# Performance work log

Measured on AMD Instinct MI355X. Metric: run time of the kernel, lower is better.

## Reference

```python
import jax, jax.numpy as jnp
import numpy as np

EMO = 1024
FEAT = 1024
K = 128  # aggregation_k
H_LIST = (4, 8, 16)
D_LIST = tuple(EMO // h for h in H_LIST)  # (256, 128, 64)
D_SUM = sum(D_LIST)  # 448
H_SUM = sum(H_LIST)  # 28
N = len(H_LIST)      # 3 subspaces
TEMP = float(np.power(D_SUM, 0.5))


def _block_mask(sizes, total):
    m = np.zeros((len(sizes), total), np.float32)
    off = 0
    for i, s in enumerate(sizes):
        m[i, off:off + s] = 1.0
        off += s
    return jnp.asarray(m)

M_Q_BLK = _block_mask(D_LIST, D_SUM)  # [N, d_sum]
M_V_BLK = _block_mask(H_LIST, H_SUM)  # [N, h_sum]


def setup_inputs() -> dict:
    key = jax.random.key(0)
    ks = iter(jax.random.split(key, 32))
    nrm = lambda shape, s=1.0: jax.random.normal(next(ks), shape, jnp.float32) * s
    B, Lt, Lp, Nv = 32, 1024, 512, 256
    return {
        "emo_embedding": nrm((B, Lt, EMO)),
        "phr_feat": nrm((B, Lp, FEAT)),
        "video_feat": nrm((B, Nv, FEAT)),
        "w_v_W": nrm((FEAT, FEAT), FEAT ** -0.5), "w_v_b": nrm((FEAT,), 0.01),
        "agg_a_W": nrm((FEAT, K), FEAT ** -0.5), "agg_a_b": nrm((K,), 0.01),
        "agg_c_W": nrm((FEAT, EMO), FEAT ** -0.5), "agg_c_b": nrm((EMO,), 0.01),
        "ele_W": nrm((2 * EMO, 1), (2 * EMO) ** -0.5), "ele_b": nrm((1,), 0.01),
        "wq_W": nrm((EMO, D_SUM), EMO ** -0.5), "wq_b": nrm((D_SUM,), 0.01),
        "wk_W": nrm((EMO, D_SUM), EMO ** -0.5), "wk_b": nrm((D_SUM,), 0.01),
        "wv_W": nrm((EMO, H_SUM), EMO ** -0.5), "wv_b": nrm((H_SUM,), 0.01),
        "wr_W": nrm((EMO, N), EMO ** -0.5), "wr_b": nrm((N,), 0.01),
    }


def reference(emo_embedding, phr_feat, video_feat,
              w_v_W, w_v_b, agg_a_W, agg_a_b, agg_c_W, agg_c_b,
              ele_W, ele_b, wq_W, wq_b, wk_W, wk_b, wv_W, wv_b, wr_W, wr_b):
    B, Lt, _ = emo_embedding.shape
    Nv = video_feat.shape[1]
    Lp = phr_feat.shape[1]

    # --- feature_aggregation ---
    # AdaptiveAvgPool1d(Nv); Lp % Nv == 0 so it is an exact reshape-mean.
    phr = phr_feat.reshape(B, Nv, Lp // Nv, FEAT).mean(axis=2)
    combine = jnp.concatenate([phr @ w_v_W + w_v_b, video_feat], axis=1)   # [B, 2*Nv, FEAT]
    attn_a = jax.nn.softmax(combine @ agg_a_W + agg_a_b, axis=-1)          # [B, 2*Nv, K]
    agg_feat = jnp.einsum('bmk,bme->bke', attn_a, combine @ agg_c_W + agg_c_b)  # [B, K, EMO]

    # --- element_routing ---
    A_pool = jnp.einsum('ble,bke->blk', emo_embedding, agg_feat).mean(axis=1)   # [B, K]
    route = jnp.einsum('bk,bke->be', A_pool, agg_feat)[:, None, :]              # [B, 1, EMO]
    route = jnp.broadcast_to(route, emo_embedding.shape)
    R_e = jnp.tanh(jnp.concatenate([emo_embedding, route], axis=-1) @ ele_W + ele_b)  # [B, Lt, 1]
    route_emo = R_e * emo_embedding                                              # [B, Lt, EMO]

    # --- subspace_routing ---
    Q = route_emo @ wq_W + wq_b        # [B, Lt, d_sum]
    Kp = agg_feat @ wk_W + wk_b        # [B, K, d_sum]
    V = agg_feat @ wv_W + wv_b         # [B, K, h_sum]
    Rp = agg_feat @ wr_W + wr_b        # [B, K, N]

    # N masked copies of Q (block subspace masks); K/R are plain repeats, V is masked.
    Qm = (Q[:, None] * M_Q_BLK[None, :, None, :]).reshape(B, N * Lt, D_SUM)
    Kf = jnp.tile(Kp, (1, N, 1))                                         # [B, N*K, d_sum]
    Vf = (V[:, None] * M_V_BLK[None, :, None, :]).reshape(B, N * K, H_SUM)
    Rf = jnp.tile(Rp, (1, N, 1))                                         # [B, N*K, N]

    attn = jax.nn.softmax(jnp.einsum('bqd,bkd->bqk', Qm, Kf) / TEMP, axis=-1)  # [B, N*Lt, N*K]
    O = jnp.tanh(attn @ Vf).reshape(B, N, Lt, H_SUM)
    O_R = (attn @ Rf).reshape(B, N, Lt, N)

    # per-subspace head gating of route_emo
    T_list = []
    hoff = 0
    for i in range(N):
        hi, di = H_LIST[i], D_LIST[i]
        ori = route_emo.reshape(B, Lt, hi, di)
        Oi = O[:, i, :, hoff:hoff + hi][..., None]      # [B, Lt, hi, 1]
        T_list.append((ori * Oi).reshape(B, Lt, EMO))
        hoff += hi
    T = jnp.stack(T_list, axis=1)                        # [B, N, Lt, EMO]

    Rdiag = jnp.stack([O_R[:, j, :, j].mean(axis=-1) for j in range(N)], axis=1)  # [B, N]
    gate = jax.nn.softmax(Rdiag, axis=-1)[:, :, None, None]
    return emo_embedding + (gate * T).sum(axis=1)
```

## Files before the change

kernel.cpp:

```cpp
#include <hip/hip_runtime.h>
#include <math.h>

typedef long long i64;
typedef __attribute__((ext_vector_type(8))) short bf16x8;
typedef __attribute__((ext_vector_type(4))) float f32x4;

#define TEMP_ISQ 0.047245559f

__device__ __forceinline__ unsigned short f2b(float x) {
  union { float f; unsigned u; } a; a.f = x;
  return (unsigned short)((a.u + 0x7fffu + ((a.u >> 16) & 1u)) >> 16);
}
__device__ __forceinline__ float b2f(unsigned short b) {
  union { float f; unsigned u; } a; a.u = ((unsigned)b) << 16; return a.f;
}

template<int BIAS, int OUTM, int RS, int BZDIV, int XMODE = 0, int SMEPI = 0>
__global__ __launch_bounds__(256)
void gemm_mfma(const unsigned short* __restrict__ Ab, i64 sA,
               const unsigned short* __restrict__ Bb, i64 sB,
               const float* __restrict__ bias,
               void* __restrict__ Ob, i64 sO,
               unsigned short* __restrict__ O2b, i64 sO2,
               int Nn, int Kd, int ldA, int ldB, int ldO,
               const float* __restrict__ rowScale, i64 sRS,
               const float* __restrict__ rsAdd)
{
  __shared__ unsigned short As[2][4096];
  __shared__ unsigned short Bs[2][4096];
  const int tid = threadIdx.x;
  const int w = tid >> 6, lane = tid & 63;

  const int gx = gridDim.x, gy = gridDim.y;
  int nwg = gx * gy * gridDim.z;
  int bid = blockIdx.x + gx * (blockIdx.y + gy * blockIdx.z);
  int L = bid;
  if ((nwg & 7) == 0) L = (bid & 7) * (nwg >> 3) + (bid >> 3);
  const int bx = L % gx;
  int rem = L / gx;
  const int by = rem % gy;
  const int z  = rem / gy;

  const int m0 = by * 128, n0 = bx * 128;
  int zA = (XMODE == 2) ? z / 3 : z;
  const unsigned short* A;
  const unsigned short* B;
  int KdL = Kd;
  if (XMODE == 3) {
    int bb = z / 3, ii = z - bb * 3;
    const int dof_[3] = {0, 256, 384};
    const int kdt_[3] = {256, 128, 64};
    A = Ab + (i64)bb * sA + dof_[ii];
    B = Bb + dof_[ii];
    KdL = kdt_[ii];
  } else if (XMODE == 2) {
    A = Ab + (i64)zA * sA;
    B = Bb + (i64)z * sB;
  } else {
    A = Ab + (i64)z * sA;
    B = Bb + (i64)(BZDIV == 1 ? z : z / BZDIV) * sB;
  }
  const int wr = w >> 1, wc = w & 1;
  const int rS = tid >> 2, sS = tid & 3;
  const int cL = lane & 15, sl = lane >> 4;

  f32x4 acc[4][4];
  #pragma unroll
  for (int i = 0; i < 4; ++i)
    #pragma unroll
    for (int j = 0; j < 4; ++j) acc[i][j] = (f32x4){0.f, 0.f, 0.f, 0.f};

  auto STAGE = [&](int buf, int k0) {
    #pragma unroll
    for (int q = 0; q < 2; ++q) {
      int r = rS + q * 64;
      int sg = sS ^ ((r >> 1) & 3);
      const unsigned short* sa = A + (i64)(m0 + r) * ldA + k0 + sg * 8;
      const unsigned short* sb = B + (i64)(n0 + r) * ldB + k0 + sg * 8;
      __builtin_amdgcn_global_load_lds(
          (__attribute__((address_space(1))) void*)sa,
          (__attribute__((address_space(3))) void*)&As[buf][r * 32 + sS * 8], 16, 0, 0);
      __builtin_amdgcn_global_load_lds(
          (__attribute__((address_space(1))) void*)sb,
          (__attribute__((address_space(3))) void*)&Bs[buf][r * 32 + sS * 8], 16, 0, 0);
    }
  };

  STAGE(0, 0);
  __syncthreads();

  for (int k0 = 0; k0 < KdL; k0 += 32) {
    const int cur = (k0 >> 5) & 1;
    if (k0 + 32 < KdL) STAGE(cur ^ 1, k0 + 32);
    bf16x8 af[4], bfv[4];
    #pragma unroll
    for (int mi = 0; mi < 4; ++mi) {
      int rr = wr * 64 + mi * 16 + cL;
      int ph = sl ^ ((rr >> 1) & 3);
      af[mi] = *(const bf16x8*)&As[cur][rr * 32 + ph * 8];
    }
    #pragma unroll
    for (int ni = 0; ni < 4; ++ni) {
      int rr = wc * 64 + ni * 16 + cL;
      int ph = sl ^ ((rr >> 1) & 3);
      bfv[ni] = *(const bf16x8*)&Bs[cur][rr * 32 + ph * 8];
    }
    #pragma unroll
    for (int mi = 0; mi < 4; ++mi)
      #pragma unroll
      for (int ni = 0; ni < 4; ++ni)
        acc[mi][ni] = __builtin_amdgcn_mfma_f32_16x16x32_bf16(af[mi], bfv[ni], acc[mi][ni], 0, 0, 0);
    __syncthreads();
  }

  const float* bp = (XMODE == 2) ? (bias + (i64)z * 128) : bias;

  if constexpr (SMEPI != 0) {
    const float scale = (SMEPI == 1) ? TEMP_ISQ : 1.f;
    #pragma unroll
    for (int mi = 0; mi < 4; ++mi)
      #pragma unroll
      for (int ni = 0; ni < 4; ++ni)
        #pragma unroll
        for (int rg = 0; rg < 4; ++rg) {
          float v = acc[mi][ni][rg];
          if (RS) v *= tanhf(rowScale[(i64)zA * sRS + m0 + wr * 64 + mi * 16 + sl * 4 + rg] + rsAdd[zA]);
          if (BIAS == 1) v += bp[wc * 64 + ni * 16 + cL];
          acc[mi][ni][rg] = v * scale;
        }
    __shared__ float smax[2][128];
    __shared__ float ssum[2][128];
    #pragma unroll
    for (int mi = 0; mi < 4; ++mi)
      #pragma unroll
      for (int rg = 0; rg < 4; ++rg) {
        float m = fmaxf(fmaxf(acc[mi][0][rg], acc[mi][1][rg]),
                        fmaxf(acc[mi][2][rg], acc[mi][3][rg]));
        #pragma unroll
        for (int o = 1; o < 16; o <<= 1) m = fmaxf(m, __shfl_xor(m, o));
        if (cL == 0) smax[wc][wr * 64 + mi * 16 + sl * 4 + rg] = m;
      }
    __syncthreads();
    #pragma unroll
    for (int mi = 0; mi < 4; ++mi)
      #pragma unroll
      for (int rg = 0; rg < 4; ++rg) {
        int r = wr * 64 + mi * 16 + sl * 4 + rg;
        float m = fmaxf(smax[0][r], smax[1][r]);
        float s = 0.f;
        #pragma unroll
        for (int ni = 0; ni < 4; ++ni) s += expf(acc[mi][ni][rg] - m);
        #pragma unroll
        for (int o = 1; o < 16; o <<= 1) s += __shfl_xor(s, o);
        if (cL == 0) ssum[wc][r] = s;
      }
    __syncthreads();
    unsigned short* OP = (unsigned short*)Ob + (i64)z * sO;
    #pragma unroll
    for (int mi = 0; mi < 4; ++mi)
      #pragma unroll
      for (int rg = 0; rg < 4; ++rg) {
        int r = wr * 64 + mi * 16 + sl * 4 + rg;
        float m = fmaxf(smax[0][r], smax[1][r]);
        float inv = 1.f / (ssum[0][r] + ssum[1][r]);
        #pragma unroll
        for (int ni = 0; ni < 4; ++ni) {
          int c = wc * 64 + ni * 16 + cL;
          unsigned short pv = f2b(expf(acc[mi][ni][rg] - m) * inv);
          if (SMEPI == 1) OP[(i64)(m0 + r) * ldO + c] = pv;
          else            OP[(i64)c * ldO + (m0 + r)] = pv;
        }
      }
    return;
  } else {
    #pragma unroll
    for (int mi = 0; mi < 4; ++mi) {
      const int rowb = m0 + wr * 64 + mi * 16 + sl * 4;
      #pragma unroll
      for (int ni = 0; ni < 4; ++ni) {
        const int col = n0 + wc * 64 + ni * 16 + cL;
        if (col < Nn) {
          float bc = (BIAS == 1) ? bp[col] : 0.f;
          #pragma unroll
          for (int rg = 0; rg < 4; ++rg) {
            float v = acc[mi][ni][rg];
            if (RS) v *= tanhf(rowScale[(i64)zA * sRS + rowb + rg] + rsAdd[zA]);
            v += bc;
            if (BIAS == 2) v += bias[rowb + rg];
            i64 oidx = (i64)(rowb + rg) * ldO + col;
            if (OUTM == 0)      ((float*)Ob)[(i64)z * sO + oidx] = v;
            else if (OUTM == 1) ((unsigned short*)Ob)[(i64)z * sO + oidx] = f2b(v);
            else if (OUTM == 3) ((float*)Ob)[(i64)z * sO + oidx] = tanhf(v * (1.f / 3.f));
            else if (OUTM == 4) {
              float ov = (col < 28) ? tanhf(v * (1.f / 3.f)) : v * (1.f / 1024.f);
              ((float*)Ob)[(i64)z * sO + oidx] = ov;
            } else {
              ((float*)Ob)[(i64)z * sO + oidx] = v;
              O2b[(i64)z * sO2 + oidx] = f2b(v);
            }
          }
        }
      }
    }
  }
}

__global__ __launch_bounds__(256)
void emo_pass1(const float* __restrict__ emo, const float* __restrict__ eleW,
               unsigned short* __restrict__ emoB, float* __restrict__ colPart,
               float* __restrict__ dotE) {
  int b = blockIdx.y, lc = blockIdx.x;
  int t = threadIdx.x, lane = t & 63, w = t >> 6;
  float4 w4 = ((const float4*)eleW)[t];
  float4 acc = make_float4(0.f, 0.f, 0.f, 0.f);
  __shared__ float dw[16][4];
  const float4* src = (const float4*)emo + ((i64)b * 1024 + lc * 16) * 256;
  ushort4* dst = (ushort4*)emoB + ((i64)b * 1024 + lc * 16) * 256;
  #pragma unroll 4
  for (int lr = 0; lr < 16; ++lr) {
    float4 v = src[lr * 256 + t];
    acc.x += v.x; acc.y += v.y; acc.z += v.z; acc.w += v.w;
    float d = v.x * w4.x + v.y * w4.y + v.z * w4.z + v.w * w4.w;
    #pragma unroll
    for (int o = 32; o; o >>= 1) d += __shfl_xor(d, o);
    if (!lane) dw[lr][w] = d;
    ushort4 o4; o4.x = f2b(v.x); o4.y = f2b(v.y); o4.z = f2b(v.z); o4.w = f2b(v.w);
    dst[lr * 256 + t] = o4;
  }
  __syncthreads();
  if (t < 16) dotE[(i64)b * 1024 + lc * 16 + t] = dw[t][0] + dw[t][1] + dw[t][2] + dw[t][3];
  ((float4*)colPart)[((i64)b * 64 + lc) * 256 + t] = acc;
}

__global__ __launch_bounds__(256)
void transpose_all(const float* __restrict__ w_v_W, const float* __restrict__ agg_a_W,
                   const float* __restrict__ agg_c_W, const float* __restrict__ wq_W,
                   const float* __restrict__ wk_W, const float* __restrict__ wv_W,
                   const float* __restrict__ wr_W,
                   unsigned short* __restrict__ wvT, unsigned short* __restrict__ aaT,
                   unsigned short* __restrict__ acT, unsigned short* __restrict__ wqB,
                   unsigned short* __restrict__ kvrT) {
  int bx = blockIdx.x;
  int t = threadIdx.x;
  if (bx >= 84) {
    i64 li = (((i64)(bx - 84) * 32 + blockIdx.y) * 256 + t) * 4;
    float4 v = *(const float4*)(wq_W + li);
    ushort4 o; o.x = f2b(v.x); o.y = f2b(v.y); o.z = f2b(v.z); o.w = f2b(v.w);
    *(ushort4*)(wqB + li) = o;
    return;
  }
  __shared__ float T[32][33];
  const float* in; unsigned short* out; int N, Npad, s0;
  if (bx < 32)      { in = w_v_W;   out = wvT;                     N = 1024; Npad = 1024; s0 = 0; }
  else if (bx < 36) { in = agg_a_W; out = aaT;                     N = 128;  Npad = 128;  s0 = 32; }
  else if (bx < 68) { in = agg_c_W; out = acT;                     N = 1024; Npad = 1024; s0 = 36; }
  else if (bx < 82) { in = wk_W;    out = kvrT;                    N = 448;  Npad = 448;  s0 = 68; }
  else if (bx < 83) { in = wv_W;    out = kvrT + (i64)448 * 1024;  N = 28;   Npad = 28;   s0 = 82; }
  else              { in = wr_W;    out = kvrT + (i64)476 * 1024;  N = 3;    Npad = 36;   s0 = 83; }
  int n0 = (bx - s0) * 32, k0 = blockIdx.y * 32;
  #pragma unroll
  for (int p = 0; p < 4; ++p) {
    int idx = t + 256 * p; int kk = idx >> 5, nn = idx & 31;
    float v = 0.f;
    if (n0 + nn < N) v = in[(i64)(k0 + kk) * N + (n0 + nn)];
    T[nn][kk] = v;
  }
  __syncthreads();
  #pragma unroll
  for (int p = 0; p < 4; ++p) {
    int idx = t + 256 * p; int nn = idx >> 5, kk = idx & 31;
    if (n0 + nn < Npad) out[(i64)(n0 + nn) * 1024 + (k0 + kk)] = f2b(T[nn][kk]);
  }
}

__global__ void kvr_bias_kernel(const float* wkb, const float* wvb, const float* wrb, float* out) {
  int t = blockIdx.x * 256 + threadIdx.x;
  if (t >= 480) return;
  out[t] = (t < 448) ? wkb[t] : (t < 476) ? wvb[t - 448] : (t < 479) ? wrb[t - 476] : 0.f;
}

__global__ void pv_conv(const float* __restrict__ phr, const float* __restrict__ video,
                        unsigned short* __restrict__ pooled, unsigned short* __restrict__ combine) {
  i64 idx = (i64)blockIdx.x * 256 + threadIdx.x;
  if (idx < 2097152) {
    i64 bm = idx >> 8; int c = (int)(idx & 255);
    i64 b = bm >> 8, m = bm & 255;
    const float4* r0 = (const float4*)(phr + (b * 512 + 2 * m) * 1024) + c;
    const float4* r1 = (const float4*)(phr + (b * 512 + 2 * m + 1) * 1024) + c;
    float4 a = *r0, d = *r1;
    ushort4 o;
    o.x = f2b(0.5f * (a.x + d.x)); o.y = f2b(0.5f * (a.y + d.y));
    o.z = f2b(0.5f * (a.z + d.z)); o.w = f2b(0.5f * (a.w + d.w));
    ((ushort4*)pooled)[idx] = o;
  } else {
    i64 j = idx - 2097152;
    i64 b = j >> 16, r = j & 65535;
    float4 v = ((const float4*)video)[j];
    ushort4 o;
    o.x = f2b(v.x); o.y = f2b(v.y); o.z = f2b(v.z); o.w = f2b(v.w);
    ((ushort4*)combine)[b * 131072 + 65536 + r] = o;
  }
}

__global__ void vtq_fill(const unsigned short* __restrict__ KVR, const float* __restrict__ wq_b,
                         unsigned short* __restrict__ VT, float* __restrict__ qb) {
  int b = blockIdx.y, bx = blockIdx.x, t = threadIdx.x;
  if (bx < 64) {
    int idx = bx * 256 + t;
    int n = idx >> 7, k = idx & 127;
    unsigned short v = 0;
    if (n < 28)      v = KVR[(i64)b * 61440 + k * 480 + 448 + n];
    else if (n < 31) v = KVR[(i64)b * 61440 + k * 480 + 476 + (n - 28)];
    VT[((i64)b * 128 + n) * 128 + k] = v;
  } else if (t < 128) {
    int ii = bx - 64;
    const int dof_[3] = {0, 256, 384};
    const int kdt_[3] = {256, 128, 64};
    const unsigned short* kp = KVR + (i64)b * 61440 + t * 480 + dof_[ii];
    const float* wb = wq_b + dof_[ii];
    float s = 0.f;
    for (int d = 0; d < kdt_[ii]; ++d) s += b2f(kp[d]) * wb[d];
    qb[(b * 3 + ii) * 128 + t] = s;
  }
}

__global__ __launch_bounds__(256)
void colmean_apool(const float* __restrict__ colPart, const float* __restrict__ aggF,
                   float* __restrict__ Apool) {
  int b = blockIdx.x, t = threadIdx.x, lane = t & 63, w = t >> 6;
  __shared__ float em[1024];
  float4 s = make_float4(0.f, 0.f, 0.f, 0.f);
  const float4* cp = (const float4*)colPart + (i64)b * 64 * 256 + t;
  for (int lc = 0; lc < 64; ++lc) {
    float4 v = cp[lc * 256];
    s.x += v.x; s.y += v.y; s.z += v.z; s.w += v.w;
  }
  em[t * 4 + 0] = s.x * (1.f / 1024.f); em[t * 4 + 1] = s.y * (1.f / 1024.f);
  em[t * 4 + 2] = s.z * (1.f / 1024.f); em[t * 4 + 3] = s.w * (1.f / 1024.f);
  __syncthreads();
  for (int k = w; k < 128; k += 4) {
    const float* ag = aggF + ((i64)b * 128 + k) * 1024;
    float d = 0.f;
    #pragma unroll
    for (int j = 0; j < 16; ++j) { int e = j * 64 + lane; d += em[e] * ag[e]; }
    #pragma unroll
    for (int o = 32; o; o >>= 1) d += __shfl_down(d, o);
    if (!lane) Apool[b * 128 + k] = d;
  }
}

__global__ __launch_bounds__(256)
void route_rb(const float* __restrict__ Apool, const float* __restrict__ aggF,
              const float* __restrict__ eleW, const float* __restrict__ eleb,
              float* __restrict__ rbv) {
  int b = blockIdx.x, t = threadIdx.x;
  __shared__ float Ap[128];
  if (t < 128) Ap[t] = Apool[b * 128 + t];
  __syncthreads();
  float4 r = make_float4(0.f, 0.f, 0.f, 0.f);
  const float4* ag = (const float4*)(aggF + (i64)b * 128 * 1024) + t;
  #pragma unroll 8
  for (int k = 0; k < 128; ++k) {
    float a = Ap[k];
    float4 v = ag[(i64)k * 256];
    r.x += a * v.x; r.y += a * v.y; r.z += a * v.z; r.w += a * v.w;
  }
  float4 w4 = ((const float4*)(eleW + 1024))[t];
  float d = r.x * w4.x + r.y * w4.y + r.z * w4.z + r.w * w4.w;
  __shared__ float red[256];
  red[t] = d; __syncthreads();
  for (int o = 128; o > 0; o >>= 1) { if (t < o) red[t] += red[t + o]; __syncthreads(); }
  if (t == 0) rbv[b] = red[0] + eleb[0];
}

__global__ void gate_kernel(const float* __restrict__ O, float* __restrict__ gate) {
  int b = blockIdx.x, t = threadIdx.x;
  __shared__ float red[128];
  __shared__ float rd[3];
  for (int i = 0; i < 3; ++i) {
    const float* op = O + ((i64)(b * 3 + i) * 1024) * 32 + 28 + i;
    float s = 0.f;
    #pragma unroll
    for (int l = t; l < 1024; l += 128) s += op[(i64)l * 32];
    red[t] = s; __syncthreads();
    for (int o = 64; o > 0; o >>= 1) { if (t < o) red[t] += red[t + o]; __syncthreads(); }
    if (t == 0) rd[i] = red[0];
    __syncthreads();
  }
  if (t == 0) {
    float m = fmaxf(rd[0], fmaxf(rd[1], rd[2]));
    float e0 = expf(rd[0] - m), e1 = expf(rd[1] - m), e2 = expf(rd[2] - m);
    float inv = 1.f / (e0 + e1 + e2);
    gate[b * 3 + 0] = e0 * inv; gate[b * 3 + 1] = e1 * inv; gate[b * 3 + 2] = e2 * inv;
  }
}

__global__ __launch_bounds__(256)
void final_kernel(const unsigned short* __restrict__ emoB, const float* __restrict__ dotE,
                  const float* __restrict__ rbv, const float* __restrict__ O,
                  const float* __restrict__ gate, float* __restrict__ out) {
  i64 bl = blockIdx.x;
  int b = (int)(bl >> 10), l = (int)(bl & 1023);
  __shared__ float Gg[16];
  int t = threadIdx.x;
  if (t < 16) {
    float g0 = gate[b * 3], g1 = gate[b * 3 + 1], g2 = gate[b * 3 + 2];
    float o0 = O[((i64)(b * 3 + 0) * 1024 + l) * 32 + (t >> 2)];
    float o1 = O[((i64)(b * 3 + 1) * 1024 + l) * 32 + 4 + (t >> 1)];
    float o2 = O[((i64)(b * 3 + 2) * 1024 + l) * 32 + 12 + t];
    Gg[t] = g0 * o0 + g1 * o1 + g2 * o2;
  }
  __syncthreads();
  float re = tanhf(dotE[bl] + rbv[b]);
  ushort4 e4 = ((const ushort4*)(emoB + bl * 1024))[t];
  float g = 1.f + re * Gg[t >> 4];
  ((float4*)(out + bl * 1024))[t] =
      make_float4(b2f(e4.x) * g, b2f(e4.y) * g, b2f(e4.z) * g, b2f(e4.w) * g);
}

extern "C" void kernel_launch(void* const* d_in, const int* in_sizes, int n_in,
                              void* d_out, int out_size, void* d_ws, size_t ws_size,
                              hipStream_t stream) {
  const float* emo     = (const float*)d_in[0];
  const float* phr     = (const float*)d_in[1];
  const float* video   = (const float*)d_in[2];
  const float* w_v_W   = (const float*)d_in[3];
  const float* w_v_b   = (const float*)d_in[4];
  const float* agg_a_W = (const float*)d_in[5];
  const float* agg_a_b = (const float*)d_in[6];
  const float* agg_c_W = (const float*)d_in[7];
  const float* agg_c_b = (const float*)d_in[8];
  const float* ele_W   = (const float*)d_in[9];
  const float* ele_b   = (const float*)d_in[10];
  const float* wq_W    = (const float*)d_in[11];
  const float* wq_b    = (const float*)d_in[12];
  const float* wk_W    = (const float*)d_in[13];
  const float* wk_b    = (const float*)d_in[14];
  const float* wv_W    = (const float*)d_in[15];
  const float* wv_b    = (const float*)d_in[16];
  const float* wr_W    = (const float*)d_in[17];
  const float* wr_b    = (const float*)d_in[18];

  char* ws = (char*)d_ws;
  const i64 oEmoB    = 0;
  const i64 oCombine = 67108864;
  const i64 oP       = 67108864;
  const i64 oPooled  = 100663296;
  const i64 oAggF    = 100663296;
  const i64 oO       = 100663296;
  const i64 oCT      = 117440512;
  const i64 oW2T     = 117440512;
  const i64 oAttnAT  = 150994944;
  const i64 oAggB    = 155189248;
  const i64 oWvT     = 163577856;
  const i64 oAaT     = 165675008;
  const i64 oAcT     = 165937152;
  const i64 oWqB     = 168034304;
  const i64 oKvrT    = 169082880;
  const i64 oKVR     = 170131456;
  const i64 oVT      = 174063616;
  const i64 oKvrB    = 175112192;
  const i64 oColPart = 175247360;
  const i64 oDotE    = 183635968;
  const i64 oApool   = 183767040;
  const i64 oQb      = 183783424;
  const i64 oRb      = 183914496;
  const i64 oGate    = 184307968;

  unsigned short* emoB    = (unsigned short*)(ws + oEmoB);
  unsigned short* combine = (unsigned short*)(ws + oCombine);
  unsigned short* P       = (unsigned short*)(ws + oP);
  unsigned short* pooled  = (unsigned short*)(ws + oPooled);
  float*          aggF    = (float*)(ws + oAggF);
  float*          O       = (float*)(ws + oO);
  unsigned short* CT      = (unsigned short*)(ws + oCT);
  unsigned short* W2T     = (unsigned short*)(ws + oW2T);
  unsigned short* attnAT  = (unsigned short*)(ws + oAttnAT);
  unsigned short* aggB    = (unsigned short*)(ws + oAggB);
  unsigned short* wvT     = (unsigned short*)(ws + oWvT);
  unsigned short* aaT     = (unsigned short*)(ws + oAaT);
  unsigned short* acT     = (unsigned short*)(ws + oAcT);
  unsigned short* wqB     = (unsigned short*)(ws + oWqB);
  unsigned short* kvrT    = (unsigned short*)(ws + oKvrT);
  unsigned short* KVR     = (unsigned short*)(ws + oKVR);
  unsigned short* VT      = (unsigned short*)(ws + oVT);
  float*          kvrB    = (float*)(ws + oKvrB);
  float*          colPart = (float*)(ws + oColPart);
  float*          dotE    = (float*)(ws + oDotE);
  float*          Apool   = (float*)(ws + oApool);
  float*          qb      = (float*)(ws + oQb);
  float*          rbv     = (float*)(ws + oRb);
  float*          gate    = (float*)(ws + oGate);

  dim3 blk(256);

  emo_pass1<<<dim3(64, 32), blk, 0, stream>>>(emo, ele_W, emoB, colPart, dotE);

  transpose_all<<<dim3(98, 32), blk, 0, stream>>>(w_v_W, agg_a_W, agg_c_W, wq_W, wk_W, wv_W, wr_W,
                                                  wvT, aaT, acT, wqB, kvrT);
  kvr_bias_kernel<<<2, blk, 0, stream>>>(wk_b, wv_b, wr_b, kvrB);

  pv_conv<<<16384, blk, 0, stream>>>(phr, video, pooled, combine);
  gemm_mfma<1, 1, 0, 1><<<dim3(8, 2, 32), blk, 0, stream>>>(pooled, 262144, wvT, 0, w_v_b,
      (void*)combine, 524288, nullptr, 0, 1024, 1024, 1024, 1024, 1024, nullptr, 0, nullptr);
  gemm_mfma<1, 1, 0, 1, 0, 2><<<dim3(1, 4, 32), blk, 0, stream>>>(combine, 524288, aaT, 0, agg_a_b,
      (void*)attnAT, 65536, nullptr, 0, 128, 1024, 1024, 1024, 512, nullptr, 0, nullptr);
  gemm_mfma<2, 1, 0, 1><<<dim3(4, 8, 32), blk, 0, stream>>>(acT, 0, combine, 524288, agg_c_b,
      (void*)CT, 524288, nullptr, 0, 512, 1024, 1024, 1024, 512, nullptr, 0, nullptr);
  gemm_mfma<0, 2, 0, 1><<<dim3(8, 1, 32), blk, 0, stream>>>(attnAT, 65536, CT, 524288, nullptr,
      (void*)aggF, 131072, aggB, 131072, 1024, 512, 512, 512, 1024, nullptr, 0, nullptr);

  colmean_apool<<<32, blk, 0, stream>>>(colPart, aggF, Apool);
  route_rb<<<32, blk, 0, stream>>>(Apool, aggF, ele_W, ele_b, rbv);

  gemm_mfma<1, 1, 0, 1><<<dim3(4, 1, 32), blk, 0, stream>>>(aggB, 131072, kvrT, 0, kvrB,
      (void*)KVR, 61440, nullptr, 0, 480, 1024, 1024, 1024, 480, nullptr, 0, nullptr);
  vtq_fill<<<dim3(67, 32), blk, 0, stream>>>(KVR, wq_b, VT, qb);

  gemm_mfma<0, 1, 0, 1, 3><<<dim3(8, 1, 96), blk, 0, stream>>>(KVR, 61440, wqB, 0, nullptr,
      (void*)W2T, 131072, nullptr, 0, 1024, 0, 480, 448, 1024, nullptr, 0, nullptr);

  gemm_mfma<1, 1, 1, 1, 2, 1><<<dim3(1, 8, 96), blk, 0, stream>>>(emoB, 1048576, W2T, 131072, qb,
      (void*)P, 131072, nullptr, 0, 128, 1024, 1024, 1024, 128, dotE, 1024, rbv);

  gemm_mfma<0, 4, 0, 3><<<dim3(1, 8, 96), blk, 0, stream>>>(P, 131072, VT, 16384, nullptr,
      (void*)O, 32768, nullptr, 0, 31, 128, 128, 128, 32, nullptr, 0, nullptr);

  gate_kernel<<<32, 128, 0, stream>>>(O, gate);
  final_kernel<<<32768, blk, 0, stream>>>(emoB, dotE, rbv, O, gate, (float*)d_out);
}
```

Baseline: 476.9 us.

## Fold w_v projection into aggregation weights and split softmax out of GEMM epilogue

Precomputes the product of the agg_c weights with the w_v weights, plus folded biases, so the pooled phrase features feed the aggregation GEMMs directly. This removes the separate w_v GEMM and the combined intermediate buffer, at the cost of an extra weight-by-weight GEMM and serial bias-folding loops. The batched GEMMs now choose A or B operands and output offsets per z-slice to handle the phrase and video halves. Separately, the fused softmax epilogue of the score GEMM is replaced by a plain bf16 store followed by a standalone softmax kernel. That adds one extra round trip of the score matrix through memory and another rounding to bf16 before the softmax.

```diff
diff --git a/kernel.cpp b/kernel.cpp
--- a/kernel.cpp
+++ b/kernel.cpp
@@ -19,7 +19,9 @@
 __global__ __launch_bounds__(256)
 void gemm_mfma(const unsigned short* __restrict__ Ab, i64 sA,
                const unsigned short* __restrict__ Bb, i64 sB,
-               const float* __restrict__ bias,
+               const unsigned short* __restrict__ Ab2,
+               const unsigned short* __restrict__ Bb2,
+               const float* __restrict__ bias, const float* __restrict__ bias2,
                void* __restrict__ Ob, i64 sO,
                unsigned short* __restrict__ O2b, i64 sO2,
                int Nn, int Kd, int ldA, int ldB, int ldO,
@@ -43,6 +45,7 @@
 
   const int m0 = by * 128, n0 = bx * 128;
   int zA = (XMODE == 2) ? z / 3 : z;
+  int zOut = z, colOff = 0, mOff = 0;
   const unsigned short* A;
   const unsigned short* B;
   int KdL = Kd;
@@ -56,10 +59,24 @@
   } else if (XMODE == 2) {
     A = Ab + (i64)zA * sA;
     B = Bb + (i64)z * sB;
+  } else if (XMODE == 5) {
+    A = Ab + (i64)z * sA;
+    B = (z >= 32) ? Bb2 : Bb;
+    zOut = z & 31;
+    mOff = (z >= 32) ? 256 : 0;
+  } else if (XMODE == 6) {
+    A = (z >= 32) ? Ab2 : Ab;
+    B = Bb + (i64)z * sB;
+    zOut = z & 31;
+    colOff = (z >= 32) ? 256 : 0;
   } else {
     A = Ab + (i64)z * sA;
     B = Bb + (i64)(BZDIV == 1 ? z : z / BZDIV) * sB;
   }
+  const float* bcol = (XMODE == 2) ? (bias + (i64)z * 128)
+                    : ((XMODE == 5 && z >= 32) ? bias2 : bias);
+  const float* brow = (XMODE == 6 && z >= 32) ? bias2 : bias;
+
   const int wr = w >> 1, wc = w & 1;
   const int rS = tid >> 2, sS = tid & 3;
   const int cL = lane & 15, sl = lane >> 4;
@@ -113,10 +130,7 @@
     __syncthreads();
   }
 
-  const float* bp = (XMODE == 2) ? (bias + (i64)z * 128) : bias;
-
-  if constexpr (SMEPI != 0) {
-    const float scale = (SMEPI == 1) ? TEMP_ISQ : 1.f;
+  if constexpr (SMEPI == 2) {
     #pragma unroll
     for (int mi = 0; mi < 4; ++mi)
       #pragma unroll
@@ -124,9 +138,8 @@
         #pragma unroll
         for (int rg = 0; rg < 4; ++rg) {
           float v = acc[mi][ni][rg];
-          if (RS) v *= tanhf(rowScale[(i64)zA * sRS + m0 + wr * 64 + mi * 16 + sl * 4 + rg] + rsAdd[zA]);
-          if (BIAS == 1) v += bp[wc * 64 + ni * 16 + cL];
-          acc[mi][ni][rg] = v * scale;
+          if (BIAS == 1) v += bcol[wc * 64 + ni * 16 + cL];
+          acc[mi][ni][rg] = v;
         }
     __shared__ float smax[2][128];
     __shared__ float ssum[2][128];
@@ -155,7 +168,7 @@
         if (cL == 0) ssum[wc][r] = s;
       }
     __syncthreads();
-    unsigned short* OP = (unsigned short*)Ob + (i64)z * sO;
+    unsigned short* OP = (unsigned short*)Ob + (i64)zOut * sO;
     #pragma unroll
     for (int mi = 0; mi < 4; ++mi)
       #pragma unroll
@@ -166,9 +179,7 @@
         #pragma unroll
         for (int ni = 0; ni < 4; ++ni) {
           int c = wc * 64 + ni * 16 + cL;
-          unsigned short pv = f2b(expf(acc[mi][ni][rg] - m) * inv);
-          if (SMEPI == 1) OP[(i64)(m0 + r) * ldO + c] = pv;
-          else            OP[(i64)c * ldO + (m0 + r)] = pv;
+          OP[(i64)c * ldO + mOff + m0 + r] = f2b(expf(acc[mi][ni][rg] - m) * inv);
         }
       }
     return;
@@ -180,23 +191,23 @@
       for (int ni = 0; ni < 4; ++ni) {
         const int col = n0 + wc * 64 + ni * 16 + cL;
         if (col < Nn) {
-          float bc = (BIAS == 1) ? bp[col] : 0.f;
+          float bc = (BIAS == 1) ? bcol[col] : 0.f;
           #pragma unroll
           for (int rg = 0; rg < 4; ++rg) {
             float v = acc[mi][ni][rg];
             if (RS) v *= tanhf(rowScale[(i64)zA * sRS + rowb + rg] + rsAdd[zA]);
             v += bc;
-            if (BIAS == 2) v += bias[rowb + rg];
-            i64 oidx = (i64)(rowb + rg) * ldO + col;
-            if (OUTM == 0)      ((float*)Ob)[(i64)z * sO + oidx] = v;
-            else if (OUTM == 1) ((unsigned short*)Ob)[(i64)z * sO + oidx] = f2b(v);
-            else if (OUTM == 3) ((float*)Ob)[(i64)z * sO + oidx] = tanhf(v * (1.f / 3.f));
+            if (BIAS == 2) v += brow[rowb + rg];
+            i64 oidx = (i64)(rowb + rg) * ldO + colOff + col;
+            if (OUTM == 0)      ((float*)Ob)[(i64)zOut * sO + oidx] = v;
+            else if (OUTM == 1) ((unsigned short*)Ob)[(i64)zOut * sO + oidx] = f2b(v);
+            else if (OUTM == 3) ((float*)Ob)[(i64)zOut * sO + oidx] = tanhf(v * (1.f / 3.f));
             else if (OUTM == 4) {
               float ov = (col < 28) ? tanhf(v * (1.f / 3.f)) : v * (1.f / 1024.f);
-              ((float*)Ob)[(i64)z * sO + oidx] = ov;
+              ((float*)Ob)[(i64)zOut * sO + oidx] = ov;
             } else {
-              ((float*)Ob)[(i64)z * sO + oidx] = v;
-              O2b[(i64)z * sO2 + oidx] = f2b(v);
+              ((float*)Ob)[(i64)zOut * sO + oidx] = v;
+              O2b[(i64)zOut * sO2 + oidx] = f2b(v);
             }
           }
         }
@@ -233,30 +244,32 @@
 }
 
 __global__ __launch_bounds__(256)
-void transpose_all(const float* __restrict__ w_v_W, const float* __restrict__ agg_a_W,
-                   const float* __restrict__ agg_c_W, const float* __restrict__ wq_W,
+void transpose_all(const float* __restrict__ agg_a_W, const float* __restrict__ agg_c_W,
+                   const float* __restrict__ wq_W, const float* __restrict__ w_v_W,
                    const float* __restrict__ wk_W, const float* __restrict__ wv_W,
                    const float* __restrict__ wr_W,
-                   unsigned short* __restrict__ wvT, unsigned short* __restrict__ aaT,
-                   unsigned short* __restrict__ acT, unsigned short* __restrict__ wqB,
+                   unsigned short* __restrict__ aaT, unsigned short* __restrict__ acT,
+                   unsigned short* __restrict__ wqB, unsigned short* __restrict__ wvB,
                    unsigned short* __restrict__ kvrT) {
   int bx = blockIdx.x;
   int t = threadIdx.x;
-  if (bx >= 84) {
-    i64 li = (((i64)(bx - 84) * 32 + blockIdx.y) * 256 + t) * 4;
-    float4 v = *(const float4*)(wq_W + li);
+  if (bx >= 52) {
+    const float* in; unsigned short* out; int base;
+    if (bx < 66) { in = wq_W;  out = wqB; base = bx - 52; }
+    else         { in = w_v_W; out = wvB; base = bx - 66; }
+    i64 li = (((i64)base * 32 + blockIdx.y) * 256 + t) * 4;
+    float4 v = *(const float4*)(in + li);
     ushort4 o; o.x = f2b(v.x); o.y = f2b(v.y); o.z = f2b(v.z); o.w = f2b(v.w);
-    *(ushort4*)(wqB + li) = o;
+    *(ushort4*)(out + li) = o;
     return;
   }
   __shared__ float T[32][33];
   const float* in; unsigned short* out; int N, Npad, s0;
-  if (bx < 32)      { in = w_v_W;   out = wvT;                     N = 1024; Npad = 1024; s0 = 0; }
-  else if (bx < 36) { in = agg_a_W; out = aaT;                     N = 128;  Npad = 128;  s0 = 32; }
-  else if (bx < 68) { in = agg_c_W; out = acT;                     N = 1024; Npad = 1024; s0 = 36; }
-  else if (bx < 82) { in = wk_W;    out = kvrT;                    N = 448;  Npad = 448;  s0 = 68; }
-  else if (bx < 83) { in = wv_W;    out = kvrT + (i64)448 * 1024;  N = 28;   Npad = 28;   s0 = 82; }
-  else              { in = wr_W;    out = kvrT + (i64)476 * 1024;  N = 3;    Npad = 36;   s0 = 83; }
+  if (bx < 4)       { in = agg_a_W; out = aaT;                     N = 128;  Npad = 128;  s0 = 0; }
+  else if (bx < 36) { in = agg_c_W; out = acT;                     N = 1024; Npad = 1024; s0 = 4; }
+  else if (bx < 50) { in = wk_W;    out = kvrT;                    N = 448;  Npad = 448;  s0 = 36; }
+  else if (bx < 51) { in = wv_W;    out = kvrT + (i64)448 * 1024;  N = 28;   Npad = 28;   s0 = 50; }
+  else              { in = wr_W;    out = kvrT + (i64)476 * 1024;  N = 3;    Npad = 36;   s0 = 51; }
   int n0 = (bx - s0) * 32, k0 = blockIdx.y * 32;
   #pragma unroll
   for (int p = 0; p < 4; ++p) {
@@ -273,14 +286,30 @@
   }
 }
 
-__global__ void kvr_bias_kernel(const float* wkb, const float* wvb, const float* wrb, float* out) {
-  int t = blockIdx.x * 256 + threadIdx.x;
-  if (t >= 480) return;
-  out[t] = (t < 448) ? wkb[t] : (t < 476) ? wvb[t - 448] : (t < 479) ? wrb[t - 476] : 0.f;
+__global__ void bias_prep(const float* wkb, const float* wvb, const float* wrb,
+                          const float* __restrict__ agg_c_W, const float* agg_c_b,
+                          const float* __restrict__ agg_a_W, const float* agg_a_b,
+                          const float* __restrict__ w_v_b,
+                          float* kvrB, float* cbrow, float* ab2) {
+  int bx = blockIdx.x, t = threadIdx.x;
+  if (bx < 2) {
+    int i = bx * 256 + t;
+    if (i < 480)
+      kvrB[i] = (i < 448) ? wkb[i] : (i < 476) ? wvb[i - 448] : (i < 479) ? wrb[i - 476] : 0.f;
+  } else if (bx < 6) {
+    int e = (bx - 2) * 256 + t;
+    float s = agg_c_b[e];
+    for (int f = 0; f < 1024; ++f) s += w_v_b[f] * agg_c_W[(i64)f * 1024 + e];
+    cbrow[e] = s;
+  } else if (t < 128) {
+    float s = agg_a_b[t];
+    for (int f = 0; f < 1024; ++f) s += w_v_b[f] * agg_a_W[(i64)f * 128 + t];
+    ab2[t] = s;
+  }
 }
 
 __global__ void pv_conv(const float* __restrict__ phr, const float* __restrict__ video,
-                        unsigned short* __restrict__ pooled, unsigned short* __restrict__ combine) {
+                        unsigned short* __restrict__ pooled, unsigned short* __restrict__ videoB) {
   i64 idx = (i64)blockIdx.x * 256 + threadIdx.x;
   if (idx < 2097152) {
     i64 bm = idx >> 8; int c = (int)(idx & 255);
@@ -294,11 +323,10 @@
     ((ushort4*)pooled)[idx] = o;
   } else {
     i64 j = idx - 2097152;
-    i64 b = j >> 16, r = j & 65535;
     float4 v = ((const float4*)video)[j];
     ushort4 o;
     o.x = f2b(v.x); o.y = f2b(v.y); o.z = f2b(v.z); o.w = f2b(v.w);
-    ((ushort4*)combine)[b * 131072 + 65536 + r] = o;
+    ((ushort4*)videoB)[j] = o;
   }
 }
 
@@ -322,6 +350,24 @@
     for (int d = 0; d < kdt_[ii]; ++d) s += b2f(kp[d]) * wb[d];
     qb[(b * 3 + ii) * 128 + t] = s;
   }
+}
+
+__global__ void softmax_P_bf(const unsigned short* __restrict__ PL, unsigned short* __restrict__ P) {
+  i64 gw = ((i64)blockIdx.x * blockDim.x + threadIdx.x) >> 6;
+  int lane = threadIdx.x & 63;
+  if (gw >= 98304) return;
+  const unsigned short* p = PL + gw * 128;
+  float x0 = b2f(p[lane]) * TEMP_ISQ, x1 = b2f(p[lane + 64]) * TEMP_ISQ;
+  float mx = fmaxf(x0, x1);
+  #pragma unroll
+  for (int o = 32; o; o >>= 1) mx = fmaxf(mx, __shfl_xor(mx, o));
+  float e0 = expf(x0 - mx), e1 = expf(x1 - mx);
+  float s = e0 + e1;
+  #pragma unroll
+  for (int o = 32; o; o >>= 1) s += __shfl_xor(s, o);
+  float inv = 1.f / s;
+  P[gw * 128 + lane] = f2b(e0 * inv);
+  P[gw * 128 + lane + 64] = f2b(e1 * inv);
 }
 
 __global__ __launch_bounds__(256)
@@ -443,23 +489,23 @@
 
   char* ws = (char*)d_ws;
   const i64 oEmoB    = 0;
-  const i64 oCombine = 67108864;
+  const i64 oPooled  = 67108864;
+  const i64 oVideoB  = 83886080;
   const i64 oP       = 67108864;
-  const i64 oPooled  = 100663296;
+  const i64 oWvB     = 100663296;
+  const i64 oW3cat   = 102760448;
   const i64 oAggF    = 100663296;
   const i64 oO       = 100663296;
   const i64 oCT      = 117440512;
   const i64 oW2T     = 117440512;
   const i64 oAttnAT  = 150994944;
   const i64 oAggB    = 155189248;
-  const i64 oWvT     = 163577856;
-  const i64 oAaT     = 165675008;
-  const i64 oAcT     = 165937152;
+  const i64 oAcaT    = 165675008;
   const i64 oWqB     = 168034304;
   const i64 oKvrT    = 169082880;
   const i64 oKVR     = 170131456;
   const i64 oVT      = 174063616;
-  const i64 oKvrB    = 175112192;
+  const i64 oBias    = 175112192;
   const i64 oColPart = 175247360;
   const i64 oDotE    = 183635968;
   const i64 oApool   = 183767040;
@@ -468,23 +514,27 @@
   const i64 oGate    = 184307968;
 
   unsigned short* emoB    = (unsigned short*)(ws + oEmoB);
-  unsigned short* combine = (unsigned short*)(ws + oCombine);
+  unsigned short* pooled  = (unsigned short*)(ws + oPooled);
+  unsigned short* videoB  = (unsigned short*)(ws + oVideoB);
   unsigned short* P       = (unsigned short*)(ws + oP);
-  unsigned short* pooled  = (unsigned short*)(ws + oPooled);
+  unsigned short* wvB     = (unsigned short*)(ws + oWvB);
+  unsigned short* W3      = (unsigned short*)(ws + oW3cat);
+  unsigned short* A2T     = W3 + (i64)1024 * 1024;
   float*          aggF    = (float*)(ws + oAggF);
   float*          O       = (float*)(ws + oO);
   unsigned short* CT      = (unsigned short*)(ws + oCT);
   unsigned short* W2T     = (unsigned short*)(ws + oW2T);
   unsigned short* attnAT  = (unsigned short*)(ws + oAttnAT);
   unsigned short* aggB    = (unsigned short*)(ws + oAggB);
-  unsigned short* wvT     = (unsigned short*)(ws + oWvT);
-  unsigned short* aaT     = (unsigned short*)(ws + oAaT);
-  unsigned short* acT     = (unsigned short*)(ws + oAcT);
+  unsigned short* acT     = (unsigned short*)(ws + oAcaT);
+  unsigned short* aaT     = acT + (i64)1024 * 1024;
   unsigned short* wqB     = (unsigned short*)(ws + oWqB);
   unsigned short* kvrT    = (unsigned short*)(ws + oKvrT);
   unsigned short* KVR     = (unsigned short*)(ws + oKVR);
   unsigned short* VT      = (unsigned short*)(ws + oVT);
-  float*          kvrB    = (float*)(ws + oKvrB);
+  float*          kvrB    = (float*)(ws + oBias);
+  float*          cbrow   = (float*)(ws + oBias + 2048);
+  float*          ab2     = (float*)(ws + oBias + 6144);
   float*          colPart = (float*)(ws + oColPart);
   float*          dotE    = (float*)(ws + oDotE);
   float*          Apool   = (float*)(ws + oApool);
@@ -496,35 +546,50 @@
 
   emo_pass1<<<dim3(64, 32), blk, 0, stream>>>(emo, ele_W, emoB, colPart, dotE);
 
-  transpose_all<<<dim3(98, 32), blk, 0, stream>>>(w_v_W, agg_a_W, agg_c_W, wq_W, wk_W, wv_W, wr_W,
-                                                  wvT, aaT, acT, wqB, kvrT);
-  kvr_bias_kernel<<<2, blk, 0, stream>>>(wk_b, wv_b, wr_b, kvrB);
-
-  pv_conv<<<16384, blk, 0, stream>>>(phr, video, pooled, combine);
-  gemm_mfma<1, 1, 0, 1><<<dim3(8, 2, 32), blk, 0, stream>>>(pooled, 262144, wvT, 0, w_v_b,
-      (void*)combine, 524288, nullptr, 0, 1024, 1024, 1024, 1024, 1024, nullptr, 0, nullptr);
-  gemm_mfma<1, 1, 0, 1, 0, 2><<<dim3(1, 4, 32), blk, 0, stream>>>(combine, 524288, aaT, 0, agg_a_b,
-      (void*)attnAT, 65536, nullptr, 0, 128, 1024, 1024, 1024, 512, nullptr, 0, nullptr);
-  gemm_mfma<2, 1, 0, 1><<<dim3(4, 8, 32), blk, 0, stream>>>(acT, 0, combine, 524288, agg_c_b,
-      (void*)CT, 524288, nullptr, 0, 512, 1024, 1024, 1024, 512, nullptr, 0, nullptr);
-  gemm_mfma<0, 2, 0, 1><<<dim3(8, 1, 32), blk, 0, stream>>>(attnAT, 65536, CT, 524288, nullptr,
-      (void*)aggF, 131072, aggB, 131072, 1024, 512, 512, 512, 1024, nullptr, 0, nullptr);
+  transpose_all<<<dim3(98, 32), blk, 0, stream>>>(agg_a_W, agg_c_W, wq_W, w_v_W,
+                                                  wk_W, wv_W, wr_W, aaT, acT, wqB, wvB, kvrT);
+  bias_prep<<<7, blk, 0, stream>>>(wk_b, wv_b, wr_b, agg_c_W, agg_c_b,
+                                   agg_a_W, agg_a_b, w_v_b, kvrB, cbrow, ab2);
+
+  pv_conv<<<16384, blk, 0, stream>>>(phr, video, pooled, videoB);
+
+  gemm_mfma<0, 1, 0, 1><<<dim3(8, 9, 1), blk, 0, stream>>>(acT, 0, wvB, 0,
+      nullptr, nullptr, nullptr, nullptr, (void*)W3, 0, nullptr, 0,
+      1024, 1024, 1024, 1024, 1024, nullptr, 0, nullptr);
+
+  gemm_mfma<2, 1, 0, 1, 6><<<dim3(2, 8, 64), blk, 0, stream>>>(W3, 0, pooled, 262144,
+      acT, nullptr, cbrow, agg_c_b, (void*)CT, 524288, nullptr, 0,
+      256, 1024, 1024, 1024, 512, nullptr, 0, nullptr);
+
+  gemm_mfma<1, 1, 0, 1, 5, 2><<<dim3(1, 2, 64), blk, 0, stream>>>(pooled, 262144, A2T, 0,
+      nullptr, aaT, ab2, agg_a_b, (void*)attnAT, 65536, nullptr, 0,
+      128, 1024, 1024, 1024, 512, nullptr, 0, nullptr);
+
+  gemm_mfma<0, 2, 0, 1><<<dim3(8, 1, 32), blk, 0, stream>>>(attnAT, 65536, CT, 524288,
+      nullptr, nullptr, nullptr, nullptr, (void*)aggF, 131072, aggB, 131072,
+      1024, 512, 512, 512, 1024, nullptr, 0, nullptr);
 
   colmean_apool<<<32, blk, 0, stream>>>(colPart, aggF, Apool);
   route_rb<<<32, blk, 0, stream>>>(Apool, aggF, ele_W, ele_b, rbv);
 
-  gemm_mfma<1, 1, 0, 1><<<dim3(4, 1, 32), blk, 0, stream>>>(aggB, 131072, kvrT, 0, kvrB,
-      (void*)KVR, 61440, nullptr, 0, 480, 1024, 1024, 1024, 480, nullptr, 0, nullptr);
+  gemm_mfma<1, 1, 0, 1><<<dim3(4, 1, 32), blk, 0, stream>>>(aggB, 131072, kvrT, 0,
+      nullptr, nullptr, kvrB, nullptr, (void*)KVR, 61440, nullptr, 0,
+      480, 1024, 1024, 1024, 480, nullptr, 0, nullptr);
   vtq_fill<<<dim3(67, 32), blk, 0, stream>>>(KVR, wq_b, VT, qb);
 
-  gemm_mfma<0, 1, 0, 1, 3><<<dim3(8, 1, 96), blk, 0, stream>>>(KVR, 61440, wqB, 0, nullptr,
-      (void*)W2T, 131072, nullptr, 0, 1024, 0, 480, 448, 1024, nullptr, 0, nullptr);
-
-  gemm_mfma<1, 1, 1, 1, 2, 1><<<dim3(1, 8, 96), blk, 0, stream>>>(emoB, 1048576, W2T, 131072, qb,
-      (void*)P, 131072, nullptr, 0, 128, 1024, 1024, 1024, 128, dotE, 1024, rbv);
-
-  gemm_mfma<0, 4, 0, 3><<<dim3(1, 8, 96), blk, 0, stream>>>(P, 131072, VT, 16384, nullptr,
-      (void*)O, 32768, nullptr, 0, 31, 128, 128, 128, 32, nullptr, 0, nullptr);
+  gemm_mfma<0, 1, 0, 1, 3><<<dim3(8, 1, 96), blk, 0, stream>>>(KVR, 61440, wqB, 0,
+      nullptr, nullptr, nullptr, nullptr, (void*)W2T, 131072, nullptr, 0,
+      1024, 0, 480, 448, 1024, nullptr, 0, nullptr);
+
+  gemm_mfma<1, 1, 1, 1, 2><<<dim3(1, 8, 96), blk, 0, stream>>>(emoB, 1048576, W2T, 131072,
+      nullptr, nullptr, qb, nullptr, (void*)P, 131072, nullptr, 0,
+      128, 1024, 1024, 1024, 128, dotE, 1024, rbv);
+
+  softmax_P_bf<<<24576, blk, 0, stream>>>(P, P);
+
+  gemm_mfma<0, 4, 0, 3><<<dim3(1, 8, 96), blk, 0, stream>>>(P, 131072, VT, 16384,
+      nullptr, nullptr, nullptr, nullptr, (void*)O, 32768, nullptr, 0,
+      31, 128, 128, 128, 32, nullptr, 0, nullptr);
 
   gate_kernel<<<32, 128, 0, stream>>>(O, gate);
   final_kernel<<<32768, blk, 0, stream>>>(emoB, dotE, rbv, O, gate, (float*)d_out);
```

Result: no change. 481.5 us (+1.0%).
